# Kernel optimization log

Hardware: AMD Instinct MI355X
Metric: run time of the kernel (lower is better)

## Reference

```python
import jax, jax.numpy as jnp
import numpy as np

HIDDEN = 2048
NUM_HEADS = 16
HEAD_DIM = HIDDEN // NUM_HEADS  # 128
BATCH = 2
SEQ = 2048
ROPE_BASE = 10000.0


def _rope_cos_sin(seq_len, dim):
    inv_freq = 1.0 / (ROPE_BASE ** (jnp.arange(0, dim, 2, dtype=jnp.float32) / dim))
    t = jnp.arange(seq_len, dtype=jnp.float32)
    freqs = jnp.outer(t, inv_freq)              # [S, dim/2]
    emb = jnp.concatenate([freqs, freqs], -1)   # [S, dim]
    return jnp.cos(emb), jnp.sin(emb)


def _rotate_half(x):
    x1, x2 = jnp.split(x, 2, axis=-1)
    return jnp.concatenate([-x2, x1], axis=-1)


def setup_inputs() -> dict:
    key = jax.random.key(0)
    k1, k2, k3 = jax.random.split(key, 3)
    hidden_states = jax.random.normal(k1, (BATCH, SEQ, HIDDEN), dtype=jnp.float32)
    Wqkv = jax.random.normal(k2, (3 * HIDDEN, HIDDEN), dtype=jnp.float32) * (1.0 / np.sqrt(HIDDEN))
    Wout = jax.random.normal(k3, (HIDDEN, HIDDEN), dtype=jnp.float32) * (1.0 / np.sqrt(HIDDEN))
    causal = jnp.tril(jnp.ones((SEQ, SEQ), dtype=bool))
    attention_mask = jnp.where(causal, 0.0, -1e9).astype(jnp.float32)[None, None]  # [1,1,S,S]
    return {"hidden_states": hidden_states, "attention_mask": attention_mask,
            "Wqkv": Wqkv, "Wout": Wout}


def reference(hidden_states, attention_mask, Wqkv, Wout):
    B, S, H = hidden_states.shape
    # fused QKV projection (torch Linear: x @ W.T)
    qkv = hidden_states @ Wqkv.T                                   # [B,S,3H]
    qkv = qkv.reshape(B, S, 3, NUM_HEADS, HEAD_DIM)
    qkv = jnp.transpose(qkv, (2, 0, 3, 1, 4))                      # [3,B,nh,S,hd]
    q, k, v = qkv[0], qkv[1], qkv[2]
    # RoPE
    cos, sin = _rope_cos_sin(S, HEAD_DIM)                          # [S,hd]
    q = q * cos + _rotate_half(q) * sin
    k = k * cos + _rotate_half(k) * sin
    # attention
    scale = jnp.sqrt(jnp.float32(HEAD_DIM))
    scores = jnp.einsum('bhqd,bhkd->bhqk', q, k) / scale           # [B,nh,S,S]
    scores = scores + attention_mask
    attn = jax.nn.softmax(scores, axis=-1)
    out = jnp.einsum('bhqk,bhkd->bhqd', attn, v)                   # [B,nh,S,hd]
    out = jnp.transpose(out, (0, 2, 1, 3)).reshape(B, S, H)
    return out @ Wout.T
```

## Files before the change

kernel.cpp:

```cpp
#include <hip/hip_runtime.h>
#include <cmath>

using u16 = unsigned short;
typedef __bf16 bf16x8 __attribute__((ext_vector_type(8)));
typedef float f32x4 __attribute__((ext_vector_type(4)));
typedef u16 u16x4 __attribute__((ext_vector_type(4)));
typedef u16 u16x8 __attribute__((ext_vector_type(8)));

#define HIDDEN 2048
#define NH 16
#define HD 128
#define BATCH 2
#define SEQ 2048
#define TOKENS 4096
#define NQKV 6144
#define CSC 0.12751744f

__device__ __forceinline__ u16 f2bf(float f) {
  union { __bf16 h; u16 u; } cv; cv.h = (__bf16)f; return cv.u;
}
__device__ __forceinline__ float bf2f(u16 u) {
  union { __bf16 h; u16 u; } cv; cv.u = u; return (float)cv.h;
}
__device__ __forceinline__ void gload16(const void* g, void* l) {
  __builtin_amdgcn_global_load_lds(
      (const __attribute__((address_space(1))) unsigned int*)g,
      (__attribute__((address_space(3))) unsigned int*)l, 16, 0, 0);
}

__global__ __launch_bounds__(256) void cvt_kernel(const float* __restrict__ in,
                                                  u16* __restrict__ out, int n8) {
  int i = blockIdx.x * 256 + threadIdx.x;
  if (i >= n8) return;
  const float4* p = (const float4*)(in + (size_t)i * 8);
  float4 f0 = p[0], f1 = p[1];
  u16x8 u;
  u[0] = f2bf(f0.x); u[1] = f2bf(f0.y); u[2] = f2bf(f0.z); u[3] = f2bf(f0.w);
  u[4] = f2bf(f1.x); u[5] = f2bf(f1.y); u[6] = f2bf(f1.z); u[7] = f2bf(f1.w);
  *(u16x8*)(out + (size_t)i * 8) = u;
}

__global__ void rope_table_kernel(float* __restrict__ ct, float* __restrict__ st) {
  int idx = blockIdx.x * blockDim.x + threadIdx.x;
  if (idx >= SEQ * 64) return;
  int s = idx >> 6, i = idx & 63;
  float invf = 1.0f / powf(10000.0f, (2.0f * (float)i) / 128.0f);
  float ang = (float)s * invf;
  ct[idx] = cosf(ang);
  st[idx] = sinf(ang);
}

__global__ __launch_bounds__(256) void rope_kernel(const u16* __restrict__ qkv,
    u16* __restrict__ qb, u16* __restrict__ kb,
    const float* __restrict__ ct, const float* __restrict__ st) {
  int gid = blockIdx.x * 256 + threadIdx.x;
  int j = gid & 7;
  int h = (gid >> 3) & 15;
  int qk = (gid >> 7) & 1;
  int t = gid >> 8;
  int s = t & (SEQ - 1), b = t >> 11;
  const u16* base = qkv + (size_t)t * 4096 + qk * 2048 + h * 128 + j * 8;
  u16x8 lo = *(const u16x8*)base;
  u16x8 hi = *(const u16x8*)(base + 64);
  const float* cp = ct + s * 64 + j * 8;
  const float* sp = st + s * 64 + j * 8;
  float scl = qk ? 1.0f : CSC;
  u16x8 olo, ohi;
#pragma unroll
  for (int e = 0; e < 8; ++e) {
    float c = cp[e], sn = sp[e];
    float xl = bf2f(lo[e]), xh = bf2f(hi[e]);
    olo[e] = f2bf((xl * c - xh * sn) * scl);
    ohi[e] = f2bf((xh * c + xl * sn) * scl);
  }
  u16* dst = (qk ? kb : qb) + ((size_t)(b * NH + h) * SEQ + s) * HD + j * 8;
  *(u16x8*)dst = olo;
  *(u16x8*)(dst + 64) = ohi;
}

template <int MODE>
__global__ __launch_bounds__(256) void gemm_bf16(
    const u16* __restrict__ A, const u16* __restrict__ B,
    int M, int N, int K, float* __restrict__ C,
    u16* __restrict__ qkvout, u16* __restrict__ vtb) {
  __shared__ u16 As[128 * 64];
  __shared__ u16 Bs[128 * 64];
  const int tid = threadIdx.x;
  const int l = tid & 63, w = tid >> 6;
  const int wm = w >> 1, wn = w & 1;
  const int m0 = blockIdx.y * 128, n0 = blockIdx.x * 128;
  const int lr8 = l >> 3, lc8 = l & 7;
  const int lg = l >> 4, lm = l & 15;
  f32x4 acc[4][4] = {};

  for (int k0 = 0; k0 < K; k0 += 64) {
#pragma unroll
    for (int c4 = 0; c4 < 4; ++c4) {
      int c = w * 4 + c4;
      int row = c * 8 + lr8;
      int se = 8 * (lc8 ^ (row & 7));
      gload16(A + (size_t)(m0 + row) * K + k0 + se, As + c * 512 + l * 8);
      gload16(B + (size_t)(n0 + row) * K + k0 + se, Bs + c * 512 + l * 8);
    }
    __syncthreads();
#pragma unroll
    for (int kk = 0; kk < 2; ++kk) {
      int ko = kk * 32 + lg * 8;
      bf16x8 af[4], bfr[4];
#pragma unroll
      for (int f = 0; f < 4; ++f) {
        int m = wm * 64 + f * 16 + lm;
        af[f] = *(const bf16x8*)&As[m * 64 + (ko ^ ((m & 7) * 8))];
        int n = wn * 64 + f * 16 + lm;
        bfr[f] = *(const bf16x8*)&Bs[n * 64 + (ko ^ ((n & 7) * 8))];
      }
#pragma unroll
      for (int i = 0; i < 4; ++i)
#pragma unroll
        for (int j = 0; j < 4; ++j)
          acc[i][j] = __builtin_amdgcn_mfma_f32_16x16x32_bf16(af[i], bfr[j], acc[i][j], 0, 0, 0);
    }
    __syncthreads();
  }

#pragma unroll
  for (int i = 0; i < 4; ++i) {
    int mrow0 = m0 + wm * 64 + i * 16 + lg * 4;
#pragma unroll
    for (int j = 0; j < 4; ++j) {
      int n = n0 + wn * 64 + j * 16 + lm;
      if (MODE == 0) {
#pragma unroll
        for (int r = 0; r < 4; ++r)
          C[(size_t)(mrow0 + r) * N + n] = acc[i][j][r];
      } else {
        if (n0 < 4096) {
#pragma unroll
          for (int r = 0; r < 4; ++r)
            qkvout[(size_t)(mrow0 + r) * 4096 + n] = f2bf(acc[i][j][r]);
        } else {
          int hh = (n - 4096) >> 7, d = n & 127;
          int bb = mrow0 >> 11, s = mrow0 & 2047;
          u16x4 pv;
#pragma unroll
          for (int r = 0; r < 4; ++r) pv[r] = f2bf(acc[i][j][r]);
          *(u16x4*)(vtb + ((size_t)((bb * NH + hh) * HD + d)) * SEQ + s) = pv;
        }
      }
    }
  }
}

__global__ __launch_bounds__(256) void attn_kernel(
    const u16* __restrict__ qb, const u16* __restrict__ kb,
    const u16* __restrict__ vtb, u16* __restrict__ aob) {
  __shared__ u16 Qs[64 * 128];
  __shared__ u16 Ks[64 * 128];
  __shared__ u16 Vts[128 * 64];
  __shared__ u16 Ps[64 * 72];
  const int tid = threadIdx.x;
  const int l = tid & 63, w = tid >> 6;
  const int lg = l >> 4, lm = l & 15;
  const int bh = blockIdx.y;
  const int qt = (int)gridDim.x - 1 - (int)blockIdx.x;
  const int q0 = qt * 64;
  const u16* qbase = qb + (size_t)bh * SEQ * HD;
  const u16* kbase = kb + (size_t)bh * SEQ * HD;
  const u16* vbase = vtb + (size_t)bh * HD * SEQ;

#pragma unroll
  for (int c4 = 0; c4 < 4; ++c4) {
    int c = w * 4 + c4;
    int row = c * 4 + lg;
    int se = 8 * (lm ^ (row & 15));
    gload16(qbase + (size_t)(q0 + row) * HD + se, Qs + c * 512 + l * 8);
  }

  f32x4 o[8] = {};
  float m_r[4], l_r[4];
#pragma unroll
  for (int r = 0; r < 4; ++r) { m_r[r] = -3.0e38f; l_r[r] = 0.0f; }

  const int nkt = q0 / 64 + 1;
  for (int kt = 0; kt < nkt; ++kt) {
    const int k0 = kt * 64;
    __syncthreads();
#pragma unroll
    for (int c4 = 0; c4 < 4; ++c4) {
      int c = w * 4 + c4;
      { int row = c * 4 + lg;
        int se = 8 * (lm ^ (row & 15));
        gload16(kbase + (size_t)(k0 + row) * HD + se, Ks + c * 512 + l * 8); }
      { int row = c * 8 + (l >> 3);
        int se = 8 * ((l & 7) ^ (row & 7));
        gload16(vbase + (size_t)row * SEQ + k0 + se, Vts + c * 512 + l * 8); }
    }
    __syncthreads();

    f32x4 sc[4] = {};
    const int qrow = w * 16 + lm;
#pragma unroll
    for (int kk = 0; kk < 4; ++kk) {
      int ko = kk * 32 + lg * 8;
      bf16x8 a = *(const bf16x8*)&Qs[qrow * 128 + (ko ^ ((qrow & 15) * 8))];
#pragma unroll
      for (int fn = 0; fn < 4; ++fn) {
        int krow = fn * 16 + lm;
        bf16x8 bb = *(const bf16x8*)&Ks[krow * 128 + (ko ^ ((krow & 15) * 8))];
        sc[fn] = __builtin_amdgcn_mfma_f32_16x16x32_bf16(a, bb, sc[fn], 0, 0, 0);
      }
    }

    const int rbase = lg * 4;
    float pm[4][4];
#pragma unroll
    for (int fn = 0; fn < 4; ++fn) {
      int kg = k0 + fn * 16 + lm;
#pragma unroll
      for (int r = 0; r < 4; ++r) {
        int qg = q0 + w * 16 + rbase + r;
        pm[fn][r] = (kg > qg) ? -3.0e38f : sc[fn][r];
      }
    }
#pragma unroll
    for (int r = 0; r < 4; ++r) {
      float mt = fmaxf(fmaxf(pm[0][r], pm[1][r]), fmaxf(pm[2][r], pm[3][r]));
#pragma unroll
      for (int off = 1; off < 16; off <<= 1) mt = fmaxf(mt, __shfl_xor(mt, off, 16));
      float mnew = fmaxf(m_r[r], mt);
      float alpha = __builtin_amdgcn_exp2f(m_r[r] - mnew);
      m_r[r] = mnew;
      float ps = 0.0f;
#pragma unroll
      for (int fn = 0; fn < 4; ++fn) {
        float p = __builtin_amdgcn_exp2f(pm[fn][r] - mnew);
        ps += p;
        Ps[(w * 16 + rbase + r) * 72 + fn * 16 + lm] = f2bf(p);
      }
#pragma unroll
      for (int off = 1; off < 16; off <<= 1) ps += __shfl_xor(ps, off, 16);
      l_r[r] = l_r[r] * alpha + ps;
#pragma unroll
      for (int f8 = 0; f8 < 8; ++f8) o[f8][r] *= alpha;
    }

    const int prow = w * 16 + lm;
#pragma unroll
    for (int ks = 0; ks < 2; ++ks) {
      int ko = ks * 32 + lg * 8;
      bf16x8 pa = *(const bf16x8*)&Ps[prow * 72 + ko];
#pragma unroll
      for (int f8 = 0; f8 < 8; ++f8) {
        int d = f8 * 16 + lm;
        bf16x8 vv = *(const bf16x8*)&Vts[d * 64 + (ko ^ ((d & 7) * 8))];
        o[f8] = __builtin_amdgcn_mfma_f32_16x16x32_bf16(pa, vv, o[f8], 0, 0, 0);
      }
    }
  }

  const int b = bh >> 4, h = bh & 15;
  float inv[4];
#pragma unroll
  for (int r = 0; r < 4; ++r) inv[r] = 1.0f / l_r[r];
#pragma unroll
  for (int f8 = 0; f8 < 8; ++f8) {
    int d = h * 128 + f8 * 16 + lm;
#pragma unroll
    for (int r = 0; r < 4; ++r) {
      int s = q0 + w * 16 + lg * 4 + r;
      aob[(size_t)(b * SEQ + s) * HIDDEN + d] = f2bf(o[f8][r] * inv[r]);
    }
  }
}

extern "C" void kernel_launch(void* const* d_in, const int* in_sizes, int n_in,
                              void* d_out, int out_size, void* d_ws, size_t ws_size,
                              hipStream_t stream) {
  const float* x = (const float*)d_in[0];
  const float* Wqkv = (const float*)d_in[2];
  const float* Wout = (const float*)d_in[3];
  float* out = (float*)d_out;

  char* ws = (char*)d_ws;
  u16* xb  = (u16*)(ws + 0);
  u16* wqb = (u16*)(ws + 16777216);
  u16* wob = (u16*)(ws + 41943040);
  u16* qkv = (u16*)(ws + 50331648);
  u16* vtb = (u16*)(ws + 83886080);
  u16* aob = (u16*)(ws + 100663296);
  float* ct = (float*)(ws + 117440512);
  float* st = (float*)(ws + 117964800);
  u16* qb = xb;
  u16* kb = wqb;

  cvt_kernel<<<4096, 256, 0, stream>>>(x, xb, 1048576);
  cvt_kernel<<<6144, 256, 0, stream>>>(Wqkv, wqb, 1572864);
  cvt_kernel<<<2048, 256, 0, stream>>>(Wout, wob, 524288);
  rope_table_kernel<<<512, 256, 0, stream>>>(ct, st);

  gemm_bf16<1><<<dim3(48, 32), 256, 0, stream>>>(xb, wqb, TOKENS, NQKV, HIDDEN,
                                                 nullptr, qkv, vtb);
  rope_kernel<<<4096, 256, 0, stream>>>(qkv, qb, kb, ct, st);
  attn_kernel<<<dim3(32, 32), 256, 0, stream>>>(qb, kb, vtb, aob);
  gemm_bf16<0><<<dim3(16, 32), 256, 0, stream>>>(aob, wob, TOKENS, HIDDEN, HIDDEN,
                                                 out, nullptr, nullptr);
}
```

Before: 470.5 us.

## Fuse RoPE into QKV GEMM epilogue, double-buffer attention, merge conversions

Merges the three fp32-to-bf16 conversion launches into one kernel. The QKV GEMM now applies RoPE and the Q scale in its epilogue, using a permuted B-fragment column mapping so each lane holds both rotate-half partners, which removes the separate rope kernel and its qkv round trip. The attention kernel keeps Q in registers, double-buffers the K/V LDS tiles so the next tile loads while the current one computes, masks only on the diagonal tile, and skips the rescale unless the running max grows by more than a threshold. It also defers the row-sum reduction to the end and raises wave priority around the MFMA sections.

```diff
diff --git a/kernel.cpp b/kernel.cpp
--- a/kernel.cpp
+++ b/kernel.cpp
@@ -28,10 +28,20 @@
       (__attribute__((address_space(3))) unsigned int*)l, 16, 0, 0);
 }
 
-__global__ __launch_bounds__(256) void cvt_kernel(const float* __restrict__ in,
-                                                  u16* __restrict__ out, int n8) {
+__global__ __launch_bounds__(256) void cvt3_kernel(
+    const float* __restrict__ x, const float* __restrict__ wq,
+    const float* __restrict__ wo, u16* __restrict__ xb,
+    u16* __restrict__ wqb, u16* __restrict__ wob) {
   int i = blockIdx.x * 256 + threadIdx.x;
-  if (i >= n8) return;
+  const float* in;
+  u16* out;
+  if (i < 1048576) {
+    in = x; out = xb;
+  } else if (i < 1048576 + 1572864) {
+    i -= 1048576; in = wq; out = wqb;
+  } else {
+    i -= 1048576 + 1572864; in = wo; out = wob;
+  }
   const float4* p = (const float4*)(in + (size_t)i * 8);
   float4 f0 = p[0], f1 = p[1];
   u16x8 u;
@@ -50,39 +60,12 @@
   st[idx] = sinf(ang);
 }
 
-__global__ __launch_bounds__(256) void rope_kernel(const u16* __restrict__ qkv,
-    u16* __restrict__ qb, u16* __restrict__ kb,
-    const float* __restrict__ ct, const float* __restrict__ st) {
-  int gid = blockIdx.x * 256 + threadIdx.x;
-  int j = gid & 7;
-  int h = (gid >> 3) & 15;
-  int qk = (gid >> 7) & 1;
-  int t = gid >> 8;
-  int s = t & (SEQ - 1), b = t >> 11;
-  const u16* base = qkv + (size_t)t * 4096 + qk * 2048 + h * 128 + j * 8;
-  u16x8 lo = *(const u16x8*)base;
-  u16x8 hi = *(const u16x8*)(base + 64);
-  const float* cp = ct + s * 64 + j * 8;
-  const float* sp = st + s * 64 + j * 8;
-  float scl = qk ? 1.0f : CSC;
-  u16x8 olo, ohi;
-#pragma unroll
-  for (int e = 0; e < 8; ++e) {
-    float c = cp[e], sn = sp[e];
-    float xl = bf2f(lo[e]), xh = bf2f(hi[e]);
-    olo[e] = f2bf((xl * c - xh * sn) * scl);
-    ohi[e] = f2bf((xh * c + xl * sn) * scl);
-  }
-  u16* dst = (qk ? kb : qb) + ((size_t)(b * NH + h) * SEQ + s) * HD + j * 8;
-  *(u16x8*)dst = olo;
-  *(u16x8*)(dst + 64) = ohi;
-}
-
 template <int MODE>
 __global__ __launch_bounds__(256) void gemm_bf16(
     const u16* __restrict__ A, const u16* __restrict__ B,
     int M, int N, int K, float* __restrict__ C,
-    u16* __restrict__ qkvout, u16* __restrict__ vtb) {
+    u16* __restrict__ qbv, u16* __restrict__ kbv, u16* __restrict__ vtb,
+    const float* __restrict__ ct, const float* __restrict__ st) {
   __shared__ u16 As[128 * 64];
   __shared__ u16 Bs[128 * 64];
   const int tid = threadIdx.x;
@@ -111,7 +94,7 @@
       for (int f = 0; f < 4; ++f) {
         int m = wm * 64 + f * 16 + lm;
         af[f] = *(const bf16x8*)&As[m * 64 + (ko ^ ((m & 7) * 8))];
-        int n = wn * 64 + f * 16 + lm;
+        int n = f * 32 + wn * 16 + lm;
         bfr[f] = *(const bf16x8*)&Bs[n * 64 + (ko ^ ((n & 7) * 8))];
       }
 #pragma unroll
@@ -126,25 +109,45 @@
 #pragma unroll
   for (int i = 0; i < 4; ++i) {
     int mrow0 = m0 + wm * 64 + i * 16 + lg * 4;
-#pragma unroll
-    for (int j = 0; j < 4; ++j) {
-      int n = n0 + wn * 64 + j * 16 + lm;
-      if (MODE == 0) {
+    if (MODE == 0) {
+#pragma unroll
+      for (int j = 0; j < 4; ++j) {
+        int n = n0 + j * 32 + wn * 16 + lm;
 #pragma unroll
         for (int r = 0; r < 4; ++r)
           C[(size_t)(mrow0 + r) * N + n] = acc[i][j][r];
-      } else {
-        if (n0 < 4096) {
-#pragma unroll
-          for (int r = 0; r < 4; ++r)
-            qkvout[(size_t)(mrow0 + r) * 4096 + n] = f2bf(acc[i][j][r]);
-        } else {
-          int hh = (n - 4096) >> 7, d = n & 127;
-          int bb = mrow0 >> 11, s = mrow0 & 2047;
-          u16x4 pv;
-#pragma unroll
-          for (int r = 0; r < 4; ++r) pv[r] = f2bf(acc[i][j][r]);
-          *(u16x4*)(vtb + ((size_t)((bb * NH + hh) * HD + d)) * SEQ + s) = pv;
+      }
+    } else if (n0 >= 4096) {
+      const int hh = (n0 & 2047) >> 7;
+      const int bb = mrow0 >> 11, s = mrow0 & 2047;
+#pragma unroll
+      for (int j = 0; j < 4; ++j) {
+        int d = j * 32 + wn * 16 + lm;
+        u16x4 pv;
+#pragma unroll
+        for (int r = 0; r < 4; ++r) pv[r] = f2bf(acc[i][j][r]);
+        *(u16x4*)(vtb + ((size_t)((bb * NH + hh) * HD + d)) * SEQ + s) = pv;
+      }
+    } else {
+      const int qk = n0 >> 11;
+      const int hh = (n0 & 2047) >> 7;
+      u16* dst = qk ? kbv : qbv;
+      const float scl = qk ? 1.0f : CSC;
+#pragma unroll
+      for (int r = 0; r < 4; ++r) {
+        int t = mrow0 + r;
+        int b = t >> 11, s = t & 2047;
+        const float* cb = ct + s * 64 + wn * 16 + lm;
+        const float* sb = st + s * 64 + wn * 16 + lm;
+        float c0 = cb[0], c1 = cb[32], s0 = sb[0], s1 = sb[32];
+        u16* row = dst + ((size_t)(b * NH + hh) * SEQ + s) * HD + wn * 16 + lm;
+#pragma unroll
+        for (int j = 0; j < 4; ++j) {
+          float cv = (j & 1) ? c1 : c0;
+          float sv = (j & 1) ? s1 : s0;
+          float x = acc[i][j][r], xp = acc[i][j ^ 2][r];
+          float ov = (j < 2) ? (x * cv - xp * sv) : (x * cv + xp * sv);
+          row[j * 32] = f2bf(ov * scl);
         }
       }
     }
@@ -154,9 +157,8 @@
 __global__ __launch_bounds__(256) void attn_kernel(
     const u16* __restrict__ qb, const u16* __restrict__ kb,
     const u16* __restrict__ vtb, u16* __restrict__ aob) {
-  __shared__ u16 Qs[64 * 128];
-  __shared__ u16 Ks[64 * 128];
-  __shared__ u16 Vts[128 * 64];
+  __shared__ u16 Ks[2][64 * 128];
+  __shared__ u16 Vts[2][128 * 64];
   __shared__ u16 Ps[64 * 72];
   const int tid = threadIdx.x;
   const int l = tid & 63, w = tid >> 6;
@@ -168,83 +170,104 @@
   const u16* kbase = kb + (size_t)bh * SEQ * HD;
   const u16* vbase = vtb + (size_t)bh * HD * SEQ;
 
-#pragma unroll
-  for (int c4 = 0; c4 < 4; ++c4) {
-    int c = w * 4 + c4;
-    int row = c * 4 + lg;
-    int se = 8 * (lm ^ (row & 15));
-    gload16(qbase + (size_t)(q0 + row) * HD + se, Qs + c * 512 + l * 8);
-  }
+  const int qrow = w * 16 + lm;
+  bf16x8 qf[4];
+#pragma unroll
+  for (int kk = 0; kk < 4; ++kk)
+    qf[kk] = *(const bf16x8*)(qbase + (size_t)(q0 + qrow) * HD + kk * 32 + lg * 8);
 
   f32x4 o[8] = {};
-  float m_r[4], l_r[4];
-#pragma unroll
-  for (int r = 0; r < 4; ++r) { m_r[r] = -3.0e38f; l_r[r] = 0.0f; }
-
-  const int nkt = q0 / 64 + 1;
-  for (int kt = 0; kt < nkt; ++kt) {
+  float m_r[4], l_p[4];
+#pragma unroll
+  for (int r = 0; r < 4; ++r) { m_r[r] = -3.0e38f; l_p[r] = 0.0f; }
+
+  const int nkt = qt + 1;
+
+  auto STAGE = [&](int bsel, int kt) {
     const int k0 = kt * 64;
-    __syncthreads();
 #pragma unroll
     for (int c4 = 0; c4 < 4; ++c4) {
       int c = w * 4 + c4;
       { int row = c * 4 + lg;
         int se = 8 * (lm ^ (row & 15));
-        gload16(kbase + (size_t)(k0 + row) * HD + se, Ks + c * 512 + l * 8); }
+        gload16(kbase + (size_t)(k0 + row) * HD + se, &Ks[bsel][c * 512 + l * 8]); }
       { int row = c * 8 + (l >> 3);
         int se = 8 * ((l & 7) ^ (row & 7));
-        gload16(vbase + (size_t)row * SEQ + k0 + se, Vts + c * 512 + l * 8); }
-    }
-    __syncthreads();
+        gload16(vbase + (size_t)row * SEQ + k0 + se, &Vts[bsel][c * 512 + l * 8]); }
+    }
+  };
+
+  STAGE(0, 0);
+  __syncthreads();
+  int cur = 0;
+
+  for (int kt = 0; kt < nkt; ++kt) {
+    if (kt + 1 < nkt) STAGE(cur ^ 1, kt + 1);
 
     f32x4 sc[4] = {};
-    const int qrow = w * 16 + lm;
+    __builtin_amdgcn_s_setprio(1);
 #pragma unroll
     for (int kk = 0; kk < 4; ++kk) {
       int ko = kk * 32 + lg * 8;
-      bf16x8 a = *(const bf16x8*)&Qs[qrow * 128 + (ko ^ ((qrow & 15) * 8))];
 #pragma unroll
       for (int fn = 0; fn < 4; ++fn) {
         int krow = fn * 16 + lm;
-        bf16x8 bb = *(const bf16x8*)&Ks[krow * 128 + (ko ^ ((krow & 15) * 8))];
-        sc[fn] = __builtin_amdgcn_mfma_f32_16x16x32_bf16(a, bb, sc[fn], 0, 0, 0);
-      }
-    }
-
-    const int rbase = lg * 4;
-    float pm[4][4];
-#pragma unroll
-    for (int fn = 0; fn < 4; ++fn) {
-      int kg = k0 + fn * 16 + lm;
+        bf16x8 bb = *(const bf16x8*)&Ks[cur][krow * 128 + (ko ^ ((krow & 15) * 8))];
+        sc[fn] = __builtin_amdgcn_mfma_f32_16x16x32_bf16(qf[kk], bb, sc[fn], 0, 0, 0);
+      }
+    }
+    __builtin_amdgcn_s_setprio(0);
+
+    if (kt == nkt - 1) {
+      const int k0 = kt * 64;
+#pragma unroll
+      for (int fn = 0; fn < 4; ++fn) {
+        int kg = k0 + fn * 16 + lm;
+#pragma unroll
+        for (int r = 0; r < 4; ++r) {
+          int qg = q0 + w * 16 + lg * 4 + r;
+          if (kg > qg) sc[fn][r] = -3.0e38f;
+        }
+      }
+    }
+
+    float mt[4];
+#pragma unroll
+    for (int r = 0; r < 4; ++r) {
+      float m01 = fmaxf(sc[0][r], sc[1][r]);
+      float m23 = fmaxf(sc[2][r], sc[3][r]);
+      float v = fmaxf(m01, m23);
+#pragma unroll
+      for (int off = 1; off < 16; off <<= 1) v = fmaxf(v, __shfl_xor(v, off, 16));
+      mt[r] = v;
+    }
+    bool need = (mt[0] > m_r[0] + 8.0f) || (mt[1] > m_r[1] + 8.0f) ||
+                (mt[2] > m_r[2] + 8.0f) || (mt[3] > m_r[3] + 8.0f);
+    if (__any(need)) {
 #pragma unroll
       for (int r = 0; r < 4; ++r) {
-        int qg = q0 + w * 16 + rbase + r;
-        pm[fn][r] = (kg > qg) ? -3.0e38f : sc[fn][r];
+        float mnew = fmaxf(m_r[r], mt[r]);
+        float alpha = __builtin_amdgcn_exp2f(m_r[r] - mnew);
+        m_r[r] = mnew;
+        l_p[r] *= alpha;
+#pragma unroll
+        for (int f8 = 0; f8 < 8; ++f8) o[f8][r] *= alpha;
       }
     }
 #pragma unroll
     for (int r = 0; r < 4; ++r) {
-      float mt = fmaxf(fmaxf(pm[0][r], pm[1][r]), fmaxf(pm[2][r], pm[3][r]));
-#pragma unroll
-      for (int off = 1; off < 16; off <<= 1) mt = fmaxf(mt, __shfl_xor(mt, off, 16));
-      float mnew = fmaxf(m_r[r], mt);
-      float alpha = __builtin_amdgcn_exp2f(m_r[r] - mnew);
-      m_r[r] = mnew;
-      float ps = 0.0f;
+      float psum = 0.0f;
 #pragma unroll
       for (int fn = 0; fn < 4; ++fn) {
-        float p = __builtin_amdgcn_exp2f(pm[fn][r] - mnew);
-        ps += p;
-        Ps[(w * 16 + rbase + r) * 72 + fn * 16 + lm] = f2bf(p);
-      }
-#pragma unroll
-      for (int off = 1; off < 16; off <<= 1) ps += __shfl_xor(ps, off, 16);
-      l_r[r] = l_r[r] * alpha + ps;
-#pragma unroll
-      for (int f8 = 0; f8 < 8; ++f8) o[f8][r] *= alpha;
+        float p = __builtin_amdgcn_exp2f(sc[fn][r] - m_r[r]);
+        psum += p;
+        Ps[(w * 16 + lg * 4 + r) * 72 + fn * 16 + lm] = f2bf(p);
+      }
+      l_p[r] += psum;
     }
 
     const int prow = w * 16 + lm;
+    __builtin_amdgcn_s_setprio(1);
 #pragma unroll
     for (int ks = 0; ks < 2; ++ks) {
       int ko = ks * 32 + lg * 8;
@@ -252,16 +275,25 @@
 #pragma unroll
       for (int f8 = 0; f8 < 8; ++f8) {
         int d = f8 * 16 + lm;
-        bf16x8 vv = *(const bf16x8*)&Vts[d * 64 + (ko ^ ((d & 7) * 8))];
+        bf16x8 vv = *(const bf16x8*)&Vts[cur][d * 64 + (ko ^ ((d & 7) * 8))];
         o[f8] = __builtin_amdgcn_mfma_f32_16x16x32_bf16(pa, vv, o[f8], 0, 0, 0);
       }
     }
-  }
-
+    __builtin_amdgcn_s_setprio(0);
+
+    __syncthreads();
+    cur ^= 1;
+  }
+
+  float inv[4];
+#pragma unroll
+  for (int r = 0; r < 4; ++r) {
+    float v = l_p[r];
+#pragma unroll
+    for (int off = 1; off < 16; off <<= 1) v += __shfl_xor(v, off, 16);
+    inv[r] = 1.0f / v;
+  }
   const int b = bh >> 4, h = bh & 15;
-  float inv[4];
-#pragma unroll
-  for (int r = 0; r < 4; ++r) inv[r] = 1.0f / l_r[r];
 #pragma unroll
   for (int f8 = 0; f8 < 8; ++f8) {
     int d = h * 128 + f8 * 16 + lm;
@@ -285,23 +317,19 @@
   u16* xb  = (u16*)(ws + 0);
   u16* wqb = (u16*)(ws + 16777216);
   u16* wob = (u16*)(ws + 41943040);
-  u16* qkv = (u16*)(ws + 50331648);
+  u16* qbv = (u16*)(ws + 50331648);
+  u16* kbv = (u16*)(ws + 67108864);
   u16* vtb = (u16*)(ws + 83886080);
   u16* aob = (u16*)(ws + 100663296);
   float* ct = (float*)(ws + 117440512);
   float* st = (float*)(ws + 117964800);
-  u16* qb = xb;
-  u16* kb = wqb;
-
-  cvt_kernel<<<4096, 256, 0, stream>>>(x, xb, 1048576);
-  cvt_kernel<<<6144, 256, 0, stream>>>(Wqkv, wqb, 1572864);
-  cvt_kernel<<<2048, 256, 0, stream>>>(Wout, wob, 524288);
+
+  cvt3_kernel<<<12288, 256, 0, stream>>>(x, Wqkv, Wout, xb, wqb, wob);
   rope_table_kernel<<<512, 256, 0, stream>>>(ct, st);
 
   gemm_bf16<1><<<dim3(48, 32), 256, 0, stream>>>(xb, wqb, TOKENS, NQKV, HIDDEN,
-                                                 nullptr, qkv, vtb);
-  rope_kernel<<<4096, 256, 0, stream>>>(qkv, qb, kb, ct, st);
-  attn_kernel<<<dim3(32, 32), 256, 0, stream>>>(qb, kb, vtb, aob);
+                                                 nullptr, qbv, kbv, vtb, ct, st);
+  attn_kernel<<<dim3(32, 32), 256, 0, stream>>>(qbv, kbv, vtb, aob);
   gemm_bf16<0><<<dim3(16, 32), 256, 0, stream>>>(aob, wob, TOKENS, HIDDEN, HIDDEN,
-                                                 out, nullptr, nullptr);
-}
+                                                 out, nullptr, nullptr, nullptr, nullptr, nullptr);
+}
```

Measured after the change: 451.0 us. 4.1% less time.
